# Optimization experiments

Hardware: AMD Instinct MI355X
Metric: run time of the kernel (lower is better)

## Reference

```python
import jax, jax.numpy as jnp
import numpy as np

N_NODES = 10000
DEG = 32            # max_edges (fixed degree after padding)
CHANNELS = 16
IN_DIM = 4
BATCH = 8


def setup_inputs() -> dict:
    key = jax.random.key(0)
    k1, k2, k3 = jax.random.split(key, 3)
    E = N_NODES * DEG
    x = jax.random.normal(k1, (BATCH, N_NODES, IN_DIM), dtype=jnp.float32)
    # neighbor indices in [0, N_NODES]; index N_NODES is the padded 'useless' zero node
    edges = jax.random.randint(k2, (E,), 0, N_NODES + 1, dtype=jnp.int64)
    # torch.rand init: uniform [0,1); one weight tensor per input channel
    weights = jax.random.uniform(k3, (IN_DIM, E, CHANNELS), dtype=jnp.float32)
    return {"x": x, "edges": edges, "weights": weights}


def reference(x, edges, weights):
    B, N, in_dim = x.shape
    E = edges.shape[0]
    deg = E // N
    C = weights.shape[-1]
    # append zero 'useless node' so padding index N gathers zeros
    x_pad = jnp.concatenate([x, jnp.zeros((B, 1, in_dim), dtype=x.dtype)], axis=1)  # [B, N+1, in_dim]
    # super_edges = cat([edges]*C); viewed as [E, C] row-major (matches torch .view)
    idx = jnp.tile(edges, C).reshape(E, C)  # [E, C]
    out = jnp.zeros((B, N, C), dtype=x.dtype)
    for i in range(in_dim):  # small fixed loop over input channels (distinct weights)
        g = x_pad[:, :, i]              # [B, N+1]
        toc = g[:, idx]                 # gather -> [B, E, C]
        conv = toc * weights[i]         # per-edge weights broadcast over batch
        out = out + conv.reshape(B, N, deg, C).sum(axis=2)  # fixed-window segment sum
    return out
```

## Files before the change

kernel.cpp:

```cpp
#include <hip/hip_runtime.h>
#include <hip/hip_bf16.h>

#define N_NODES 10000
#define DEG     32
#define CH      16
#define IN_DIM  4
#define BATCH   8
#define E_EDGES (N_NODES * DEG)
#define WI_STRIDE (E_EDGES * CH)
#define P_COUNT 625
#define LX_STRIDE 36

__global__ __launch_bounds__(256) void lcg_transpose(const float* __restrict__ x,
                                                     float* __restrict__ xt) {
    int t = blockIdx.x * 256 + threadIdx.x;
    if (t < BATCH * N_NODES) {
        int b = t / N_NODES;
        int node = t - b * N_NODES;
        float4 v = *(const float4*)(x + 4 * t);
        *(float4*)(xt + node * 32 + b * 4) = v;
    } else if (t < BATCH * N_NODES + 8) {
        int r = t - BATCH * N_NODES;
        *(float4*)(xt + N_NODES * 32 + r * 4) = make_float4(0.f, 0.f, 0.f, 0.f);
    }
}

__global__ __launch_bounds__(512, 4) void lcg_main(
    const float* __restrict__ xt,
    const int*   __restrict__ edges,
    const float* __restrict__ w,
    float*       __restrict__ out)
{
    __shared__ float lx[512 * LX_STRIDE];

    int bid = blockIdx.x;
    int p   = bid >> 1;
    int jh  = bid & 1;
    int t   = threadIdx.x;

    {
        int sub = t & 7;
        int rg  = t >> 3;
        const int* ep = edges + 512 * p;
        int nd[8];
#pragma unroll
        for (int k = 0; k < 8; k++) nd[k] = ep[rg + 64 * k];
#pragma unroll
        for (int k = 0; k < 8; k++) {
            int s = rg + 64 * k;
            float4 v = *(const float4*)(xt + nd[k] * 32 + sub * 4);
            *(float4*)(&lx[s * LX_STRIDE + sub * 4]) = v;
        }
    }
    __syncthreads();

    int lane = t & 63;
    int wv   = t >> 6;
    int c    = lane & 15;
    int dq   = lane >> 4;
    int j    = 8 * jh + wv;
    int n    = p + P_COUNT * j;

    const float* wb = w + n * (DEG * CH) + lane;

    float acc[BATCH];
#pragma unroll
    for (int b = 0; b < BATCH; b++) acc[b] = 0.0f;

    const float* lrow = &lx[(16 * dq + c) * LX_STRIDE];

#pragma unroll 2
    for (int ds = 0; ds < 8; ds++) {
        float w0 = wb[64 * ds];
        float w1 = wb[64 * ds + WI_STRIDE];
        float w2 = wb[64 * ds + 2 * WI_STRIDE];
        float w3 = wb[64 * ds + 3 * WI_STRIDE];
        const float* lr = lrow + ds * (64 * LX_STRIDE);
#pragma unroll
        for (int b = 0; b < BATCH; b++) {
            float4 xq = *(const float4*)(lr + 4 * b);
            acc[b] += xq.x * w0 + xq.y * w1 + xq.z * w2 + xq.w * w3;
        }
    }

#pragma unroll
    for (int b = 0; b < BATCH; b++) {
        acc[b] += __shfl_xor(acc[b], 16, 64);
        acc[b] += __shfl_xor(acc[b], 32, 64);
    }

    int ob = n * CH + c;
    out[(2 * dq + 0) * (N_NODES * CH) + ob] = acc[2 * dq + 0];
    out[(2 * dq + 1) * (N_NODES * CH) + ob] = acc[2 * dq + 1];
}

extern "C" void kernel_launch(void* const* d_in, const int* in_sizes, int n_in,
                              void* d_out, int out_size, void* d_ws, size_t ws_size,
                              hipStream_t stream) {
    const float* x     = (const float*)d_in[0];
    const int*   edges = (const int*)d_in[1];
    const float* w     = (const float*)d_in[2];
    float* out = (float*)d_out;
    float* xt  = (float*)d_ws;

    int tr_total  = BATCH * N_NODES + 8;
    int tr_blocks = (tr_total + 255) / 256;
    lcg_transpose<<<tr_blocks, 256, 0, stream>>>(x, xt);

    lcg_main<<<2 * P_COUNT, 512, 0, stream>>>(xt, edges, w, out);
}
```

Before: 130.5 us.

## Double-buffer neighbor gathers in shared memory and prefetch weights per step

Instead of gathering all 512 neighbor rows into a large shared buffer before computing, the kernel now gathers 64 rows per step into a two-slot shared buffer. It prefetches the next step's gather and weights while computing on the current slot. This cuts shared memory per block from about 72KB to about 18KB, which can raise occupancy, and overlaps gather latency with FMA work. The cost is seven extra block-wide barriers per block, and the last iteration issues a redundant weight load.

```diff
diff --git a/kernel.cpp b/kernel.cpp
--- a/kernel.cpp
+++ b/kernel.cpp
@@ -31,35 +31,22 @@
     const float* __restrict__ w,
     float*       __restrict__ out)
 {
-    __shared__ float lx[512 * LX_STRIDE];
+    __shared__ float lx[2][64 * LX_STRIDE];
 
     int bid = blockIdx.x;
     int p   = bid >> 1;
     int jh  = bid & 1;
     int t   = threadIdx.x;
 
-    {
-        int sub = t & 7;
-        int rg  = t >> 3;
-        const int* ep = edges + 512 * p;
-        int nd[8];
-#pragma unroll
-        for (int k = 0; k < 8; k++) nd[k] = ep[rg + 64 * k];
-#pragma unroll
-        for (int k = 0; k < 8; k++) {
-            int s = rg + 64 * k;
-            float4 v = *(const float4*)(xt + nd[k] * 32 + sub * 4);
-            *(float4*)(&lx[s * LX_STRIDE + sub * 4]) = v;
-        }
-    }
-    __syncthreads();
+    int sub = t & 7;
+    int rg  = t >> 3;
+    const int* ep = edges + 512 * p;
 
     int lane = t & 63;
     int wv   = t >> 6;
     int c    = lane & 15;
     int dq   = lane >> 4;
-    int j    = 8 * jh + wv;
-    int n    = p + P_COUNT * j;
+    int n    = p + P_COUNT * (8 * jh + wv);
 
     const float* wb = w + n * (DEG * CH) + lane;
 
@@ -67,19 +54,42 @@
 #pragma unroll
     for (int b = 0; b < BATCH; b++) acc[b] = 0.0f;
 
-    const float* lrow = &lx[(16 * dq + c) * LX_STRIDE];
+    {
+        int nd0 = ep[rg];
+        float4 g0 = *(const float4*)(xt + nd0 * 32 + sub * 4);
+        *(float4*)(&lx[0][rg * LX_STRIDE + sub * 4]) = g0;
+    }
+    float wc0 = wb[0];
+    float wc1 = wb[WI_STRIDE];
+    float wc2 = wb[2 * WI_STRIDE];
+    float wc3 = wb[3 * WI_STRIDE];
+    __syncthreads();
 
-#pragma unroll 2
+#pragma unroll
     for (int ds = 0; ds < 8; ds++) {
-        float w0 = wb[64 * ds];
-        float w1 = wb[64 * ds + WI_STRIDE];
-        float w2 = wb[64 * ds + 2 * WI_STRIDE];
-        float w3 = wb[64 * ds + 3 * WI_STRIDE];
-        const float* lr = lrow + ds * (64 * LX_STRIDE);
+        int dsn = ds < 7 ? ds + 1 : 7;
+        float wn0 = wb[64 * dsn];
+        float wn1 = wb[64 * dsn + WI_STRIDE];
+        float wn2 = wb[64 * dsn + 2 * WI_STRIDE];
+        float wn3 = wb[64 * dsn + 3 * WI_STRIDE];
+
+        float4 g;
+        if (ds < 7) {
+            int nd = ep[64 * (ds + 1) + rg];
+            g = *(const float4*)(xt + nd * 32 + sub * 4);
+        }
+
+        const float* lr = &lx[ds & 1][(16 * dq + c) * LX_STRIDE];
 #pragma unroll
         for (int b = 0; b < BATCH; b++) {
             float4 xq = *(const float4*)(lr + 4 * b);
-            acc[b] += xq.x * w0 + xq.y * w1 + xq.z * w2 + xq.w * w3;
+            acc[b] += xq.x * wc0 + xq.y * wc1 + xq.z * wc2 + xq.w * wc3;
+        }
+        wc0 = wn0; wc1 = wn1; wc2 = wn2; wc3 = wn3;
+
+        if (ds < 7) {
+            *(float4*)(&lx[(ds + 1) & 1][rg * LX_STRIDE + sub * 4]) = g;
+            __syncthreads();
         }
     }
 
```

Measured after the change: 155.6 us. 1.19x slower.

## Split neighbor gather into two halves to overlap with compute

Applied to the files above, without the earlier changes.

Splits the shared-memory gather of neighbor features into two halves. The second half's global loads are issued into registers while the first half is being computed, then written to a second LDS buffer. This aims to hide gather latency behind FMA work, at the cost of extra registers and a second barrier.

```diff
diff --git a/kernel.cpp b/kernel.cpp
--- a/kernel.cpp
+++ b/kernel.cpp
@@ -31,35 +31,22 @@
     const float* __restrict__ w,
     float*       __restrict__ out)
 {
-    __shared__ float lx[512 * LX_STRIDE];
+    __shared__ float lx[2][256 * LX_STRIDE];
 
     int bid = blockIdx.x;
     int p   = bid >> 1;
     int jh  = bid & 1;
     int t   = threadIdx.x;
 
-    {
-        int sub = t & 7;
-        int rg  = t >> 3;
-        const int* ep = edges + 512 * p;
-        int nd[8];
-#pragma unroll
-        for (int k = 0; k < 8; k++) nd[k] = ep[rg + 64 * k];
-#pragma unroll
-        for (int k = 0; k < 8; k++) {
-            int s = rg + 64 * k;
-            float4 v = *(const float4*)(xt + nd[k] * 32 + sub * 4);
-            *(float4*)(&lx[s * LX_STRIDE + sub * 4]) = v;
-        }
-    }
-    __syncthreads();
+    int sub = t & 7;
+    int rg  = t >> 3;
+    const int* ep = edges + 512 * p;
 
     int lane = t & 63;
     int wv   = t >> 6;
     int c    = lane & 15;
     int dq   = lane >> 4;
-    int j    = 8 * jh + wv;
-    int n    = p + P_COUNT * j;
+    int n    = p + P_COUNT * (8 * jh + wv);
 
     const float* wb = w + n * (DEG * CH) + lane;
 
@@ -67,15 +54,50 @@
 #pragma unroll
     for (int b = 0; b < BATCH; b++) acc[b] = 0.0f;
 
-    const float* lrow = &lx[(16 * dq + c) * LX_STRIDE];
+#pragma unroll
+    for (int k = 0; k < 4; k++) {
+        int r  = rg + 64 * k;
+        int nd = ep[r];
+        float4 g = *(const float4*)(xt + nd * 32 + sub * 4);
+        *(float4*)(&lx[0][r * LX_STRIDE + sub * 4]) = g;
+    }
+    __syncthreads();
 
-#pragma unroll 2
-    for (int ds = 0; ds < 8; ds++) {
+    int ndn[4];
+#pragma unroll
+    for (int k = 0; k < 4; k++) ndn[k] = ep[256 + rg + 64 * k];
+    float4 gn[4];
+#pragma unroll
+    for (int k = 0; k < 4; k++)
+        gn[k] = *(const float4*)(xt + ndn[k] * 32 + sub * 4);
+
+#pragma unroll
+    for (int dsl = 0; dsl < 4; dsl++) {
+        float w0 = wb[64 * dsl];
+        float w1 = wb[64 * dsl + WI_STRIDE];
+        float w2 = wb[64 * dsl + 2 * WI_STRIDE];
+        float w3 = wb[64 * dsl + 3 * WI_STRIDE];
+        const float* lr = &lx[0][(64 * dsl + 16 * dq + c) * LX_STRIDE];
+#pragma unroll
+        for (int b = 0; b < BATCH; b++) {
+            float4 xq = *(const float4*)(lr + 4 * b);
+            acc[b] += xq.x * w0 + xq.y * w1 + xq.z * w2 + xq.w * w3;
+        }
+    }
+
+#pragma unroll
+    for (int k = 0; k < 4; k++)
+        *(float4*)(&lx[1][(rg + 64 * k) * LX_STRIDE + sub * 4]) = gn[k];
+    __syncthreads();
+
+#pragma unroll
+    for (int dsl = 0; dsl < 4; dsl++) {
+        int ds = 4 + dsl;
         float w0 = wb[64 * ds];
         float w1 = wb[64 * ds + WI_STRIDE];
         float w2 = wb[64 * ds + 2 * WI_STRIDE];
         float w3 = wb[64 * ds + 3 * WI_STRIDE];
-        const float* lr = lrow + ds * (64 * LX_STRIDE);
+        const float* lr = &lx[1][(64 * dsl + 16 * dq + c) * LX_STRIDE];
 #pragma unroll
         for (int b = 0; b < BATCH; b++) {
             float4 xq = *(const float4*)(lr + 4 * b);
```

Measured after the change: 129.9 us. About the same (-0.5%).
